# Optimization experiments

Measured on AMD Instinct MI355X. Metric: run time of the kernel, lower is better.

## Reference

```python
import jax, jax.numpy as jnp
import numpy as np

FS = 4096.0
TRAIN_KERNEL = 4
TRAIN_STRIDE = 0.25
BATCH = 1024
NPERSEG = 4096          # fftlength * fs
NOVERLAP = NPERSEG // 2 # default overlap
FL, FH = 20.0, 500.0


def _welch(data):
    """Faithful port of _torch_welch with average='mean' (which is a SUM over segments
    in the original code), off by the same constant factor as the original."""
    N, nsample = data.shape
    nstride = NPERSEG - NOVERLAP
    nseg = int(np.ceil((nsample - NPERSEG) / nstride)) + 1
    # frame indices [nseg, nperseg] (static numpy -> cheap gather)
    idx = np.arange(nseg)[:, None] * nstride + np.arange(NPERSEG)[None, :]
    frames = data[:, idx]                                   # [N, nseg, nperseg]
    n = np.arange(NPERSEG)
    window = (0.5 - 0.5 * np.cos(2.0 * np.pi * n / NPERSEG)).astype(np.float32) * 2.0  # periodic hann * 2
    fd = jnp.fft.rfft(frames * window, axis=-1)             # [N, nseg, nfreq]
    power = jnp.real(fd) ** 2 + jnp.imag(fd) ** 2
    psd = jnp.sum(power, axis=1)                            # original 'mean' branch uses sum
    T = nsample * FS
    return psd / T                                          # [N, nfreq]


def setup_inputs() -> dict:
    key = jax.random.key(0)
    k1, k2 = jax.random.split(key)
    T = int(TRAIN_KERNEL * FS)  # 16384
    pred = jax.random.normal(k1, (BATCH, T), dtype=jnp.float32)
    target = jax.random.normal(k2, (BATCH, T), dtype=jnp.float32)
    return {"pred": pred, "target": target}


def reference(pred, target):
    res = target - pred
    s = int(TRAIN_STRIDE * FS)                     # 1024 samples per stride
    shape_x = int(TRAIN_KERNEL / TRAIN_STRIDE)     # 16
    # cross[i] = res[:, i*s:(i+1)*s].flatten() -> reshape/transpose, no loop
    def to_cross(x):
        return x[:, : shape_x * s].reshape(BATCH, shape_x, s).transpose(1, 0, 2).reshape(shape_x, BATCH * s)
    cross_res = to_cross(res)
    cross_target = to_cross(target)

    psd_res = _welch(cross_res)                    # [shape_x, nfreq]
    psd_target = _welch(cross_target)

    nfreq = NPERSEG // 2 + 1
    freq = np.linspace(0.0, FS / 2.0, nfreq)
    mask = jnp.asarray((FL < freq) & (freq < FH))
    dfreq = float(freq[1] - freq[0])
    scale = FH - FL

    psd_res = jnp.where(mask, psd_res, 0.0)
    psd_ratio = psd_res / psd_target
    loss = jnp.sum(psd_ratio, axis=1) * dfreq / scale  # [shape_x]
    return jnp.mean(loss[-8:]) * loss.shape[0]
```

## Files before the change

### kernel.cpp

```cpp
#include <hip/hip_runtime.h>

#define NSEG 511
#define NROWS 8
#define ROW0 8
#define K0 21
#define KEND 500
#define NFREQ 479
#define ACC_STRIDE 512
#define ACC_ELEMS (2 * NROWS * ACC_STRIDE)
#define NREP 8
#define SPB 8
#define NGROUPS 64
#define NBLOCKS (2 * NROWS * NGROUPS)

__device__ __forceinline__ int sw(int i) { return i ^ (((i >> 5) & 7) << 2); }
__device__ __forceinline__ int natq(int m) { return m + 4 * ((m >> 4) & 3); }

__device__ __forceinline__ float2 cmul(float2 a, float2 b) {
    return make_float2(fmaf(a.x, b.x, -a.y * b.y), fmaf(a.x, b.y, a.y * b.x));
}
__device__ __forceinline__ float2 cadd(float2 a, float2 b) { return make_float2(a.x + b.x, a.y + b.y); }
__device__ __forceinline__ float2 csub(float2 a, float2 b) { return make_float2(a.x - b.x, a.y - b.y); }

__device__ __forceinline__ void dft8(float2& x0, float2& x1, float2& x2, float2& x3,
                                     float2& x4, float2& x5, float2& x6, float2& x7) {
    const float C45 = 0.70710678118654752440f;
    float2 t0 = cadd(x0, x4), u0 = csub(x0, x4);
    float2 t1 = cadd(x1, x5), u1 = csub(x1, x5);
    float2 t2 = cadd(x2, x6), u2 = csub(x2, x6);
    float2 t3 = cadd(x3, x7), u3 = csub(x3, x7);
    float2 s0 = cadd(t0, t2), d0 = csub(t0, t2);
    float2 s1 = cadd(t1, t3), d1 = csub(t1, t3);
    float2 v1 = make_float2(C45 * (u1.x + u1.y), C45 * (u1.y - u1.x));
    float2 v2 = make_float2(u2.y, -u2.x);
    float2 v3 = make_float2(C45 * (u3.y - u3.x), -C45 * (u3.x + u3.y));
    float2 s2 = cadd(u0, v2), d2 = csub(u0, v2);
    float2 s3 = cadd(v1, v3), d3 = csub(v1, v3);
    float2 mid1 = make_float2(d1.y, -d1.x);
    float2 mid3 = make_float2(d3.y, -d3.x);
    x0 = cadd(s0, s1); x4 = csub(s0, s1);
    x2 = cadd(d0, mid1); x6 = csub(d0, mid1);
    x1 = cadd(s2, s3); x5 = csub(s2, s3);
    x3 = cadd(d2, mid3); x7 = csub(d2, mid3);
}

__device__ __forceinline__ void twiddle8cs(float2& x1, float2& x2, float2& x3, float2& x4,
                                           float2& x5, float2& x6, float2& x7,
                                           float c, float s) {
    float2 w1 = make_float2(c, s);
    float2 w2 = cmul(w1, w1);
    float2 w3 = cmul(w2, w1);
    float2 w4 = cmul(w2, w2);
    float2 w5 = cmul(w4, w1);
    float2 w6 = cmul(w3, w3);
    float2 w7 = cmul(w4, w3);
    x1 = cmul(x1, w1); x2 = cmul(x2, w2); x3 = cmul(x3, w3);
    x4 = cmul(x4, w4); x5 = cmul(x5, w5); x6 = cmul(x6, w6);
    x7 = cmul(x7, w7);
}

__global__ __launch_bounds__(256)
void psd_kernel(const float* __restrict__ pred,
                const float* __restrict__ target,
                float* __restrict__ acc) {
    __shared__ float2 buf[2048];
    __shared__ float2 nat[2064];

    const int bid = blockIdx.x;
    const int grp = bid % NGROUPS;
    const int row = (bid / NGROUPS) % NROWS + ROW0;
    const int sig = bid / (NGROUPS * NROWS);
    const int tid = threadIdx.x;
    const int seg0 = grp * SPB;
    const int ns = (seg0 + SPB <= NSEG) ? SPB : (NSEG - seg0);

    const float2* t2p = (const float2*)target;
    const float2* p2p = (const float2*)pred;

    const int base = 2 * seg0 * 8192 + row * 512 + tid;
#define LOADRAW(X, IDX)                                                      \
    {                                                                        \
        int _i = (IDX);                                                      \
        float2 v = t2p[_i];                                                  \
        if (sig == 0) { float2 p = p2p[_i]; v.x -= p.x; v.y -= p.y; }        \
        X = v;                                                               \
    }
    float2 r0, r1, r2, r3, r4, r5, r6, r7;
    LOADRAW(r0, base)
    LOADRAW(r1, base + 256)
    LOADRAW(r2, base + 8192)
    LOADRAW(r3, base + 8448)
    LOADRAW(r4, base + 16384)
    LOADRAW(r5, base + 16640)
    LOADRAW(r6, base + 24576)
    LOADRAW(r7, base + 24832)

    const float WA = 3.06796157577128245e-3f;
    const float H  = 0.70710678118654752440f;
    float sa, ca;
    __sincosf((float)tid * WA, &sa, &ca);
    float sb, cb;
    __sincosf((float)(tid & 31) * -2.45436926061702596e-2f, &sb, &cb);
    float cc, ss;
    {
        const float TC1 = 0.98078528040323044913f, TS1 = -0.19509032201612826785f;
        const float TC2 = 0.92387953251128675613f, TS2 = -0.38268343236508977173f;
        const float TC3 = 0.83146961230254523708f, TS3 = -0.55557023301960222474f;
        int mq = tid & 3;
        cc = (mq & 2) ? ((mq & 1) ? TC3 : TC2) : ((mq & 1) ? TC1 : 1.0f);
        ss = (mq & 2) ? ((mq & 1) ? TS3 : TS2) : ((mq & 1) ? TS1 : 0.0f);
    }

    const int k1 = K0 + tid;
    const bool has2 = (tid < KEND - K0 - 256);

    float sn0, cs0;
    __sincosf(-1.53398078788564123e-3f * (float)k1, &sn0, &cs0);

    const int qk = natq(k1);
    const int qn = natq(512 - k1);

    const int mb = 8 * ((tid >> 2) & 7) + (tid >> 5);
    const int natC = natq(mb) + 513 * (tid & 3);

    float pw1 = 0.0f, pw2 = 0.0f;

    #pragma unroll 1
    for (int s = 0; s < ns; ++s) {
        const float CD = 0.99999882344642529f;
        const float SD = 1.53398018628476550e-3f;
        float cat = ca, sat = sa;
        asm volatile("" : "+v"(cat), "+v"(sat));
        float2 wv0, wv1, wv2, wv3, wv4, wv5, wv6, wv7;
#define MKW(W, CE, SE) { float cr = (CE), sr = (SE);                         \
        W = make_float2(1.0f - cr, 1.0f - (cr * CD - sr * SD)); }
        MKW(wv0, cat, sat)
        MKW(wv1, H * (cat - sat), H * (sat + cat))
        MKW(wv2, -sat, cat)
        MKW(wv3, -H * (cat + sat), H * (cat - sat))
        MKW(wv4, -cat, -sat)
        MKW(wv5, H * (sat - cat), -H * (sat + cat))
        MKW(wv6, sat, -cat)
        MKW(wv7, H * (cat + sat), H * (sat - cat))
#undef MKW

        float2 x0 = make_float2(r0.x * wv0.x, r0.y * wv0.y);
        float2 x1 = make_float2(r1.x * wv1.x, r1.y * wv1.y);
        float2 x2 = make_float2(r2.x * wv2.x, r2.y * wv2.y);
        float2 x3 = make_float2(r3.x * wv3.x, r3.y * wv3.y);
        float2 x4 = make_float2(r4.x * wv4.x, r4.y * wv4.y);
        float2 x5 = make_float2(r5.x * wv5.x, r5.y * wv5.y);
        float2 x6 = make_float2(r6.x * wv6.x, r6.y * wv6.y);
        float2 x7 = make_float2(r7.x * wv7.x, r7.y * wv7.y);

        if (s + 1 < ns) {
            r0 = r4; r1 = r5; r2 = r6; r3 = r7;
            int nb = base + (s + 1) * 16384;
            LOADRAW(r4, nb + 16384)
            LOADRAW(r5, nb + 16640)
            LOADRAW(r6, nb + 24576)
            LOADRAW(r7, nb + 24832)
        }

        dft8(x0, x1, x2, x3, x4, x5, x6, x7);
        twiddle8cs(x1, x2, x3, x4, x5, x6, x7, ca, -sa);
        buf[sw(tid)]        = x0;
        buf[sw(tid + 256)]  = x1;
        buf[sw(tid + 512)]  = x2;
        buf[sw(tid + 768)]  = x3;
        buf[sw(tid + 1024)] = x4;
        buf[sw(tid + 1280)] = x5;
        buf[sw(tid + 1536)] = x6;
        buf[sw(tid + 1792)] = x7;
        __syncthreads();

        {
            const int baseB = (tid & 31) + 256 * (tid >> 5);
            x0 = buf[sw(baseB)];
            x1 = buf[sw(baseB + 32)];
            x2 = buf[sw(baseB + 64)];
            x3 = buf[sw(baseB + 96)];
            x4 = buf[sw(baseB + 128)];
            x5 = buf[sw(baseB + 160)];
            x6 = buf[sw(baseB + 192)];
            x7 = buf[sw(baseB + 224)];
            dft8(x0, x1, x2, x3, x4, x5, x6, x7);
            twiddle8cs(x1, x2, x3, x4, x5, x6, x7, cb, sb);
            buf[sw(baseB)]       = x0;
            buf[sw(baseB + 32)]  = x1;
            buf[sw(baseB + 64)]  = x2;
            buf[sw(baseB + 96)]  = x3;
            buf[sw(baseB + 128)] = x4;
            buf[sw(baseB + 160)] = x5;
            buf[sw(baseB + 192)] = x6;
            buf[sw(baseB + 224)] = x7;
        }

        {
            const int baseC = (tid & 3) + 32 * ((tid >> 2) & 7) + 256 * (tid >> 5);
            x0 = buf[sw(baseC)];
            x1 = buf[sw(baseC + 4)];
            x2 = buf[sw(baseC + 8)];
            x3 = buf[sw(baseC + 12)];
            x4 = buf[sw(baseC + 16)];
            x5 = buf[sw(baseC + 20)];
            x6 = buf[sw(baseC + 24)];
            x7 = buf[sw(baseC + 28)];
            dft8(x0, x1, x2, x3, x4, x5, x6, x7);
            twiddle8cs(x1, x2, x3, x4, x5, x6, x7, cc, ss);
            nat[natC]       = x0;
            nat[natC + 64]  = x1;
            nat[natC + 128] = x2;
            nat[natC + 192] = x3;
            nat[natC + 256] = x4;
            nat[natC + 320] = x5;
            nat[natC + 384] = x6;
            nat[natC + 448] = x7;
        }
        __syncthreads();

        {
            float2 a0 = nat[qk],        a1 = nat[qk + 513];
            float2 a2 = nat[qk + 1026], a3 = nat[qk + 1539];
            float2 zk = make_float2((a0.x + a1.x) + (a2.x + a3.x),
                                    (a0.y + a1.y) + (a2.y + a3.y));
            float2 b0 = nat[qn],        b1 = nat[qn + 513];
            float2 b2 = nat[qn + 1026], b3 = nat[qn + 1539];
            float D0x = b0.x - b2.x, D0y = b0.y - b2.y;
            float D1x = b1.x - b3.x, D1y = b1.y - b3.y;
            float2 zn = make_float2(D0x - D1y, D0y + D1x);
            float Ex = 0.5f * (zk.x + zn.x);
            float Ey = 0.5f * (zk.y - zn.y);
            float Ox = 0.5f * (zk.y + zn.y);
            float Oy = -0.5f * (zk.x - zn.x);
            float xr = Ex + Ox * cs0 - Oy * sn0;
            float xi = Ey + Ox * sn0 + Oy * cs0;
            pw1 += xr * xr + xi * xi;
        }
        if (has2) {
            float c0 = cs0, s0 = sn0;
            asm volatile("" : "+v"(c0), "+v"(s0));
            const float CU = 0.98078528040323044913f;
            const float SU = 0.19509032201612826785f;
            float cs1 = c0 * CU + s0 * SU;
            float sn1 = s0 * CU - c0 * SU;
            float2 a0 = nat[qk + 256],  a1 = nat[qk + 769];
            float2 a2 = nat[qk + 1282], a3 = nat[qk + 1795];
            float2 zk = make_float2((a0.x + a1.x) + (a2.x + a3.x),
                                    (a0.y + a1.y) + (a2.y + a3.y));
            float2 b0 = nat[qn - 256],  b1 = nat[qn + 257];
            float2 b2 = nat[qn + 770],  b3 = nat[qn + 1283];
            float D0x = b0.x - b2.x, D0y = b0.y - b2.y;
            float D1x = b1.x - b3.x, D1y = b1.y - b3.y;
            float2 zn = make_float2(D0x - D1y, D0y + D1x);
            float Ex = 0.5f * (zk.x + zn.x);
            float Ey = 0.5f * (zk.y - zn.y);
            float Ox = 0.5f * (zk.y + zn.y);
            float Oy = -0.5f * (zk.x - zn.x);
            float xr = Ex + Ox * cs1 - Oy * sn1;
            float xi = Ey + Ox * sn1 + Oy * cs1;
            pw2 += xr * xr + xi * xi;
        }
    }

    {
        float* accR = acc + (bid & (NREP - 1)) * ACC_ELEMS;
        int i0 = (sig * NROWS + (row - ROW0)) * ACC_STRIDE;
        atomicAdd(&accR[i0 + tid], pw1);
        if (has2) atomicAdd(&accR[i0 + 256 + tid], pw2);
    }
#undef LOADRAW
}

__global__ __launch_bounds__(256)
void reduce_kernel(const float* __restrict__ acc, float* __restrict__ out) {
    __shared__ float sh[256];
    int tid = threadIdx.x;
    float sum = 0.0f;
    for (int n = tid; n < NROWS * NFREQ; n += 256) {
        int r = n / NFREQ, k = n % NFREQ;
        float num = 0.0f, den = 0.0f;
        #pragma unroll
        for (int rep = 0; rep < NREP; ++rep) {
            num += acc[rep * ACC_ELEMS + r * ACC_STRIDE + k];
            den += acc[rep * ACC_ELEMS + (NROWS + r) * ACC_STRIDE + k];
        }
        sum += num / den;
    }
    sh[tid] = sum;
    __syncthreads();
    for (int s = 128; s > 0; s >>= 1) {
        if (tid < s) sh[tid] += sh[tid + s];
        __syncthreads();
    }
    if (tid == 0) out[0] = sh[0] * (1.0f / 240.0f);
}

extern "C" void kernel_launch(void* const* d_in, const int* in_sizes, int n_in,
                              void* d_out, int out_size, void* d_ws, size_t ws_size,
                              hipStream_t stream) {
    const float* pred = (const float*)d_in[0];
    const float* target = (const float*)d_in[1];
    float* acc = (float*)d_ws;

    hipMemsetAsync(acc, 0, NREP * ACC_ELEMS * sizeof(float), stream);
    psd_kernel<<<NBLOCKS, 256, 0, stream>>>(pred, target, acc);
    reduce_kernel<<<1, 256, 0, stream>>>(acc, (float*)d_out);
}
```

Measured before the change: 163.5 us.

## Software-pipeline FFT stage A, hoist twiddle/window tables, XOR-swizzle nat buffer

```diff
diff --git a/kernel.cpp b/kernel.cpp
--- a/kernel.cpp
+++ b/kernel.cpp
@@ -14,7 +14,7 @@
 #define NBLOCKS (2 * NROWS * NGROUPS)
 
 __device__ __forceinline__ int sw(int i) { return i ^ (((i >> 5) & 7) << 2); }
-__device__ __forceinline__ int natq(int m) { return m + 4 * ((m >> 4) & 3); }
+__device__ __forceinline__ int nsw(int m) { return m ^ (((m >> 4) & 3) << 2); }
 
 __device__ __forceinline__ float2 cmul(float2 a, float2 b) {
     return make_float2(fmaf(a.x, b.x, -a.y * b.y), fmaf(a.x, b.y, a.y * b.x));
@@ -44,16 +44,21 @@
     x3 = cadd(d2, mid3); x7 = csub(d2, mid3);
 }
 
-__device__ __forceinline__ void twiddle8cs(float2& x1, float2& x2, float2& x3, float2& x4,
-                                           float2& x5, float2& x6, float2& x7,
-                                           float c, float s) {
-    float2 w1 = make_float2(c, s);
-    float2 w2 = cmul(w1, w1);
-    float2 w3 = cmul(w2, w1);
-    float2 w4 = cmul(w2, w2);
-    float2 w5 = cmul(w4, w1);
-    float2 w6 = cmul(w3, w3);
-    float2 w7 = cmul(w4, w3);
+__device__ __forceinline__ void twbuild(float c, float s,
+                                        float2& w1, float2& w2, float2& w3, float2& w4,
+                                        float2& w5, float2& w6, float2& w7) {
+    w1 = make_float2(c, s);
+    w2 = cmul(w1, w1);
+    w3 = cmul(w2, w1);
+    w4 = cmul(w2, w2);
+    w5 = cmul(w4, w1);
+    w6 = cmul(w3, w3);
+    w7 = cmul(w4, w3);
+}
+__device__ __forceinline__ void twapply(float2& x1, float2& x2, float2& x3, float2& x4,
+                                        float2& x5, float2& x6, float2& x7,
+                                        float2 w1, float2 w2, float2 w3, float2 w4,
+                                        float2 w5, float2 w6, float2 w7) {
     x1 = cmul(x1, w1); x2 = cmul(x2, w2); x3 = cmul(x3, w3);
     x4 = cmul(x4, w4); x5 = cmul(x5, w5); x6 = cmul(x6, w6);
     x7 = cmul(x7, w7);
@@ -64,7 +69,7 @@
                 const float* __restrict__ target,
                 float* __restrict__ acc) {
     __shared__ float2 buf[2048];
-    __shared__ float2 nat[2064];
+    __shared__ float2 nat[2048];
 
     const int bid = blockIdx.x;
     const int grp = bid % NGROUPS;
@@ -96,11 +101,32 @@
     LOADRAW(r7, base + 24832)
 
     const float WA = 3.06796157577128245e-3f;
+    const float CD = 0.99999882344642529f;
+    const float SD = 1.53398018628476550e-3f;
     const float H  = 0.70710678118654752440f;
     float sa, ca;
     __sincosf((float)tid * WA, &sa, &ca);
-    float sb, cb;
-    __sincosf((float)(tid & 31) * -2.45436926061702596e-2f, &sb, &cb);
+    float2 wv0, wv1, wv2, wv3, wv4, wv5, wv6, wv7;
+#define MKW(W, CE, SE) { float cr = (CE), sr = (SE);                         \
+        W = make_float2(1.0f - cr, 1.0f - (cr * CD - sr * SD)); }
+    MKW(wv0, ca, sa)
+    MKW(wv1, H * (ca - sa), H * (sa + ca))
+    MKW(wv2, -sa, ca)
+    MKW(wv3, -H * (ca + sa), H * (ca - sa))
+    MKW(wv4, -ca, -sa)
+    MKW(wv5, H * (sa - ca), -H * (sa + ca))
+    MKW(wv6, sa, -ca)
+    MKW(wv7, H * (ca + sa), H * (sa - ca))
+#undef MKW
+    float2 wA1, wA2, wA3, wA4, wA5, wA6, wA7;
+    twbuild(ca, -sa, wA1, wA2, wA3, wA4, wA5, wA6, wA7);
+    {
+        float sb, cb;
+        __sincosf((float)(tid & 31) * -2.45436926061702596e-2f, &sb, &cb);
+        sa = sb; ca = cb;
+    }
+    float2 wB1, wB2, wB3, wB4, wB5, wB6, wB7;
+    twbuild(ca, sa, wB1, wB2, wB3, wB4, wB5, wB6, wB7);
     float cc, ss;
     {
         const float TC1 = 0.98078528040323044913f, TS1 = -0.19509032201612826785f;
@@ -110,40 +136,30 @@
         cc = (mq & 2) ? ((mq & 1) ? TC3 : TC2) : ((mq & 1) ? TC1 : 1.0f);
         ss = (mq & 2) ? ((mq & 1) ? TS3 : TS2) : ((mq & 1) ? TS1 : 0.0f);
     }
+    float2 wC1, wC2, wC3, wC4, wC5, wC6, wC7;
+    twbuild(cc, ss, wC1, wC2, wC3, wC4, wC5, wC6, wC7);
 
     const int k1 = K0 + tid;
     const bool has2 = (tid < KEND - K0 - 256);
 
-    float sn0, cs0;
+    float sn0, cs0, sn1, cs1;
     __sincosf(-1.53398078788564123e-3f * (float)k1, &sn0, &cs0);
-
-    const int qk = natq(k1);
-    const int qn = natq(512 - k1);
+    {
+        const float CU = 0.98078528040323044913f;
+        const float SU = 0.19509032201612826785f;
+        cs1 = cs0 * CU + sn0 * SU;
+        sn1 = sn0 * CU - cs0 * SU;
+    }
+
+    const int qk0 = nsw(k1);
+    const int qn0 = nsw(512 - k1);
 
     const int mb = 8 * ((tid >> 2) & 7) + (tid >> 5);
-    const int natC = natq(mb) + 513 * (tid & 3);
+    const int natC = (nsw(mb) ^ (tid & 3)) + 512 * (tid & 3);
 
     float pw1 = 0.0f, pw2 = 0.0f;
 
-    #pragma unroll 1
-    for (int s = 0; s < ns; ++s) {
-        const float CD = 0.99999882344642529f;
-        const float SD = 1.53398018628476550e-3f;
-        float cat = ca, sat = sa;
-        asm volatile("" : "+v"(cat), "+v"(sat));
-        float2 wv0, wv1, wv2, wv3, wv4, wv5, wv6, wv7;
-#define MKW(W, CE, SE) { float cr = (CE), sr = (SE);                         \
-        W = make_float2(1.0f - cr, 1.0f - (cr * CD - sr * SD)); }
-        MKW(wv0, cat, sat)
-        MKW(wv1, H * (cat - sat), H * (sat + cat))
-        MKW(wv2, -sat, cat)
-        MKW(wv3, -H * (cat + sat), H * (cat - sat))
-        MKW(wv4, -cat, -sat)
-        MKW(wv5, H * (sat - cat), -H * (sat + cat))
-        MKW(wv6, sat, -cat)
-        MKW(wv7, H * (cat + sat), H * (sat - cat))
-#undef MKW
-
+    {
         float2 x0 = make_float2(r0.x * wv0.x, r0.y * wv0.y);
         float2 x1 = make_float2(r1.x * wv1.x, r1.y * wv1.y);
         float2 x2 = make_float2(r2.x * wv2.x, r2.y * wv2.y);
@@ -152,18 +168,16 @@
         float2 x5 = make_float2(r5.x * wv5.x, r5.y * wv5.y);
         float2 x6 = make_float2(r6.x * wv6.x, r6.y * wv6.y);
         float2 x7 = make_float2(r7.x * wv7.x, r7.y * wv7.y);
-
-        if (s + 1 < ns) {
+        if (ns > 1) {
             r0 = r4; r1 = r5; r2 = r6; r3 = r7;
-            int nb = base + (s + 1) * 16384;
+            int nb = base + 16384;
             LOADRAW(r4, nb + 16384)
             LOADRAW(r5, nb + 16640)
             LOADRAW(r6, nb + 24576)
             LOADRAW(r7, nb + 24832)
         }
-
         dft8(x0, x1, x2, x3, x4, x5, x6, x7);
-        twiddle8cs(x1, x2, x3, x4, x5, x6, x7, ca, -sa);
+        twapply(x1, x2, x3, x4, x5, x6, x7, wA1, wA2, wA3, wA4, wA5, wA6, wA7);
         buf[sw(tid)]        = x0;
         buf[sw(tid + 256)]  = x1;
         buf[sw(tid + 512)]  = x2;
@@ -172,20 +186,23 @@
         buf[sw(tid + 1280)] = x5;
         buf[sw(tid + 1536)] = x6;
         buf[sw(tid + 1792)] = x7;
-        __syncthreads();
-
+    }
+    __syncthreads();
+
+    #pragma unroll 1
+    for (int s = 0; s < ns; ++s) {
         {
             const int baseB = (tid & 31) + 256 * (tid >> 5);
-            x0 = buf[sw(baseB)];
-            x1 = buf[sw(baseB + 32)];
-            x2 = buf[sw(baseB + 64)];
-            x3 = buf[sw(baseB + 96)];
-            x4 = buf[sw(baseB + 128)];
-            x5 = buf[sw(baseB + 160)];
-            x6 = buf[sw(baseB + 192)];
-            x7 = buf[sw(baseB + 224)];
+            float2 x0 = buf[sw(baseB)];
+            float2 x1 = buf[sw(baseB + 32)];
+            float2 x2 = buf[sw(baseB + 64)];
+            float2 x3 = buf[sw(baseB + 96)];
+            float2 x4 = buf[sw(baseB + 128)];
+            float2 x5 = buf[sw(baseB + 160)];
+            float2 x6 = buf[sw(baseB + 192)];
+            float2 x7 = buf[sw(baseB + 224)];
             dft8(x0, x1, x2, x3, x4, x5, x6, x7);
-            twiddle8cs(x1, x2, x3, x4, x5, x6, x7, cb, sb);
+            twapply(x1, x2, x3, x4, x5, x6, x7, wB1, wB2, wB3, wB4, wB5, wB6, wB7);
             buf[sw(baseB)]       = x0;
             buf[sw(baseB + 32)]  = x1;
             buf[sw(baseB + 64)]  = x2;
@@ -198,16 +215,16 @@
 
         {
             const int baseC = (tid & 3) + 32 * ((tid >> 2) & 7) + 256 * (tid >> 5);
-            x0 = buf[sw(baseC)];
-            x1 = buf[sw(baseC + 4)];
-            x2 = buf[sw(baseC + 8)];
-            x3 = buf[sw(baseC + 12)];
-            x4 = buf[sw(baseC + 16)];
-            x5 = buf[sw(baseC + 20)];
-            x6 = buf[sw(baseC + 24)];
-            x7 = buf[sw(baseC + 28)];
+            float2 x0 = buf[sw(baseC)];
+            float2 x1 = buf[sw(baseC + 4)];
+            float2 x2 = buf[sw(baseC + 8)];
+            float2 x3 = buf[sw(baseC + 12)];
+            float2 x4 = buf[sw(baseC + 16)];
+            float2 x5 = buf[sw(baseC + 20)];
+            float2 x6 = buf[sw(baseC + 24)];
+            float2 x7 = buf[sw(baseC + 28)];
             dft8(x0, x1, x2, x3, x4, x5, x6, x7);
-            twiddle8cs(x1, x2, x3, x4, x5, x6, x7, cc, ss);
+            twapply(x1, x2, x3, x4, x5, x6, x7, wC1, wC2, wC3, wC4, wC5, wC6, wC7);
             nat[natC]       = x0;
             nat[natC + 64]  = x1;
             nat[natC + 128] = x2;
@@ -219,13 +236,46 @@
         }
         __syncthreads();
 
+        if (s + 1 < ns) {
+            float2 x0 = make_float2(r0.x * wv0.x, r0.y * wv0.y);
+            float2 x1 = make_float2(r1.x * wv1.x, r1.y * wv1.y);
+            float2 x2 = make_float2(r2.x * wv2.x, r2.y * wv2.y);
+            float2 x3 = make_float2(r3.x * wv3.x, r3.y * wv3.y);
+            float2 x4 = make_float2(r4.x * wv4.x, r4.y * wv4.y);
+            float2 x5 = make_float2(r5.x * wv5.x, r5.y * wv5.y);
+            float2 x6 = make_float2(r6.x * wv6.x, r6.y * wv6.y);
+            float2 x7 = make_float2(r7.x * wv7.x, r7.y * wv7.y);
+            if (s + 2 < ns) {
+                r0 = r4; r1 = r5; r2 = r6; r3 = r7;
+                int nb = base + (s + 2) * 16384;
+                LOADRAW(r4, nb + 16384)
+                LOADRAW(r5, nb + 16640)
+                LOADRAW(r6, nb + 24576)
+                LOADRAW(r7, nb + 24832)
+            }
+            dft8(x0, x1, x2, x3, x4, x5, x6, x7);
+            twapply(x1, x2, x3, x4, x5, x6, x7, wA1, wA2, wA3, wA4, wA5, wA6, wA7);
+            buf[sw(tid)]        = x0;
+            buf[sw(tid + 256)]  = x1;
+            buf[sw(tid + 512)]  = x2;
+            buf[sw(tid + 768)]  = x3;
+            buf[sw(tid + 1024)] = x4;
+            buf[sw(tid + 1280)] = x5;
+            buf[sw(tid + 1536)] = x6;
+            buf[sw(tid + 1792)] = x7;
+        }
+
         {
-            float2 a0 = nat[qk],        a1 = nat[qk + 513];
-            float2 a2 = nat[qk + 1026], a3 = nat[qk + 1539];
+            float2 a0 = nat[qk0];
+            float2 a1 = nat[(qk0 ^ 1) + 512];
+            float2 a2 = nat[(qk0 ^ 2) + 1024];
+            float2 a3 = nat[(qk0 ^ 3) + 1536];
             float2 zk = make_float2((a0.x + a1.x) + (a2.x + a3.x),
                                     (a0.y + a1.y) + (a2.y + a3.y));
-            float2 b0 = nat[qn],        b1 = nat[qn + 513];
-            float2 b2 = nat[qn + 1026], b3 = nat[qn + 1539];
+            float2 b0 = nat[qn0];
+            float2 b1 = nat[(qn0 ^ 1) + 512];
+            float2 b2 = nat[(qn0 ^ 2) + 1024];
+            float2 b3 = nat[(qn0 ^ 3) + 1536];
             float D0x = b0.x - b2.x, D0y = b0.y - b2.y;
             float D1x = b1.x - b3.x, D1y = b1.y - b3.y;
             float2 zn = make_float2(D0x - D1y, D0y + D1x);
@@ -238,18 +288,16 @@
             pw1 += xr * xr + xi * xi;
         }
         if (has2) {
-            float c0 = cs0, s0 = sn0;
-            asm volatile("" : "+v"(c0), "+v"(s0));
-            const float CU = 0.98078528040323044913f;
-            const float SU = 0.19509032201612826785f;
-            float cs1 = c0 * CU + s0 * SU;
-            float sn1 = s0 * CU - c0 * SU;
-            float2 a0 = nat[qk + 256],  a1 = nat[qk + 769];
-            float2 a2 = nat[qk + 1282], a3 = nat[qk + 1795];
+            float2 a0 = nat[qk0 + 256];
+            float2 a1 = nat[(qk0 ^ 1) + 768];
+            float2 a2 = nat[(qk0 ^ 2) + 1280];
+            float2 a3 = nat[(qk0 ^ 3) + 1792];
             float2 zk = make_float2((a0.x + a1.x) + (a2.x + a3.x),
                                     (a0.y + a1.y) + (a2.y + a3.y));
-            float2 b0 = nat[qn - 256],  b1 = nat[qn + 257];
-            float2 b2 = nat[qn + 770],  b3 = nat[qn + 1283];
+            float2 b0 = nat[qn0 - 256];
+            float2 b1 = nat[(qn0 ^ 1) + 256];
+            float2 b2 = nat[(qn0 ^ 2) + 768];
+            float2 b3 = nat[(qn0 ^ 3) + 1280];
             float D0x = b0.x - b2.x, D0y = b0.y - b2.y;
             float D1x = b1.x - b3.x, D1y = b1.y - b3.y;
             float2 zn = make_float2(D0x - D1y, D0y + D1x);
@@ -261,6 +309,7 @@
             float xi = Ey + Ox * sn1 + Oy * cs1;
             pw2 += xr * xr + xi * xi;
         }
+        if (s + 1 < ns) __syncthreads();
     }
 
     {
```

New measurement: 161.4 us. Within noise of the previous version (-1.3%).
